# Performance work log

Measured on AMD Instinct MI355X. Metric: run time of the kernel, lower is better.

## Reference

```python
import jax, jax.numpy as jnp
import numpy as np

B, S, D = 4, 2048, 1024
H, HD = 16, 64  # n_heads, head_dim (n_kv_heads == n_heads -> n_rep = 1)
WINDOW = 256
ROPE_THETA = 10000.0


def setup_inputs() -> dict:
    key = jax.random.key(0)
    ks = jax.random.split(key, 5)
    x = jax.random.normal(ks[0], (B, S, D), dtype=jnp.float32)
    scale = 0.02
    wq = jax.random.normal(ks[1], (D, D), dtype=jnp.float32) * scale
    wk = jax.random.normal(ks[2], (D, D), dtype=jnp.float32) * scale
    wv = jax.random.normal(ks[3], (D, D), dtype=jnp.float32) * scale
    wo = jax.random.normal(ks[4], (D, D), dtype=jnp.float32) * scale
    # RoPE frequencies: freqs_cis[t, i] = exp(1j * t / theta^(2i/HD)), i in [0, HD/2)
    inv_freq = 1.0 / (ROPE_THETA ** (jnp.arange(0, HD, 2, dtype=jnp.float32) / HD))
    t = jnp.arange(S, dtype=jnp.float32)
    ang = t[:, None] * inv_freq[None, :]  # [S, HD/2]
    return {"x": x, "freqs_cos": jnp.cos(ang), "freqs_sin": jnp.sin(ang),
            "wq": wq, "wk": wk, "wv": wv, "wo": wo}


def _apply_rope(xq, xk, cos, sin):
    # xq/xk: [B, S, H, HD]; cos/sin: [S, HD/2] broadcast as [1, S, 1, HD/2]
    def rot(v):
        vr = v.reshape(*v.shape[:-1], HD // 2, 2)
        v0, v1 = vr[..., 0], vr[..., 1]
        c = cos[None, :, None, :]
        s = sin[None, :, None, :]
        o0 = v0 * c - v1 * s
        o1 = v0 * s + v1 * c
        return jnp.stack([o0, o1], axis=-1).reshape(v.shape)
    return rot(xq), rot(xk)


def reference(x, freqs_cos, freqs_sin, wq, wk, wv, wo):
    b, s, _ = x.shape
    xq = (x @ wq.T).reshape(b, s, H, HD)
    xk = (x @ wk.T).reshape(b, s, H, HD)
    xv = (x @ wv.T).reshape(b, s, H, HD)
    xq, xk = _apply_rope(xq, xk, freqs_cos, freqs_sin)
    # [B, H, S, S] scores
    scores = jnp.einsum('bqhd,bkhd->bhqk', xq, xk) / jnp.sqrt(jnp.float32(HD))
    pos = jnp.arange(s)
    # masked (disallowed) when j > i (future) or i - j >= window
    bad = (pos[None, :] > pos[:, None]) | (pos[:, None] - pos[None, :] >= WINDOW)
    scores = jnp.where(bad[None, None], -jnp.inf, scores)
    attn = jax.nn.softmax(scores.astype(jnp.float32), axis=-1).astype(xq.dtype)
    out = jnp.einsum('bhqk,bkhd->bqhd', attn, xv).reshape(b, s, H * HD)
    return out @ wo.T
```

## Files before the change

kernel.cpp:

```cpp
#include <hip/hip_runtime.h>
#include <hip/hip_bf16.h>


typedef __bf16 bf16_t;
typedef __attribute__((ext_vector_type(8))) __bf16 bf16x8;
typedef __attribute__((ext_vector_type(4))) __bf16 bf16x4;
typedef __attribute__((ext_vector_type(4))) float f32x4;

#define MFMA16(a, b, c) __builtin_amdgcn_mfma_f32_16x16x32_bf16((a), (b), (c), 0, 0, 0)

__device__ __forceinline__ void async16(const void* g, void* l) {
    __builtin_amdgcn_global_load_lds(
        (const __attribute__((address_space(1))) unsigned int*)g,
        (__attribute__((address_space(3))) unsigned int*)l, 16, 0, 0);
}

#define BAR() do { asm volatile("" ::: "memory"); __builtin_amdgcn_s_barrier(); \
                   asm volatile("" ::: "memory"); } while (0)
#define VMC(N) asm volatile("s_waitcnt vmcnt(" #N ")" ::: "memory")

__global__ __launch_bounds__(256) void cvt_kernel(const float* __restrict__ s,
                                                  bf16_t* __restrict__ d, int n) {
    int i = (blockIdx.x * 256 + threadIdx.x) * 8;
    if (i >= n) return;
    float4 a = *(const float4*)(s + i);
    float4 b = *(const float4*)(s + i + 4);
    bf16x8 o;
    o[0] = (bf16_t)a.x; o[1] = (bf16_t)a.y; o[2] = (bf16_t)a.z; o[3] = (bf16_t)a.w;
    o[4] = (bf16_t)b.x; o[5] = (bf16_t)b.y; o[6] = (bf16_t)b.z; o[7] = (bf16_t)b.w;
    *(bf16x8*)(d + i) = o;
}

template <typename OUT>
__global__ __launch_bounds__(512, 2) void gemm256(const bf16_t* __restrict__ A,
                                                  const bf16_t* __restrict__ Bw,
                                                  OUT* __restrict__ C,
                                                  int M, int N, int K) {
    __shared__ __attribute__((aligned(16))) bf16_t As[49152];
    __shared__ __attribute__((aligned(16))) bf16_t Bs[24576];
    const int tid = threadIdx.x;
    const int l = tid & 63, w = tid >> 6;
    const int lr = l & 15, lg = l >> 4;
    const int wr = w >> 1, wc = w & 1;

    const int nwg = gridDim.x * gridDim.y;
    const int flat = blockIdx.y * gridDim.x + blockIdx.x;
    const int swz = (flat & 7) * (nwg >> 3) + (flat >> 3);
    const int bx = swz % gridDim.x, by = swz / gridDim.x;
    const long m0 = (long)by * 256, n0 = (long)bx * 128;
    const int NT = K >> 6;

    int rS[2], cS[2];
#pragma unroll
    for (int i = 0; i < 2; ++i) {
        const int p  = i * 8192 + w * 1024 + l * 16;
        const int pp = p ^ (((p >> 9) & 1) << 5);
        const int st = pp >> 10;
        rS[i] = (st >> 1) * 16 + ((pp >> 6) & 15);
        cS[i] = (st & 1) * 32 + ((pp >> 4) & 3) * 8;
    }
    const bf16_t* aSrc0 = A  + (m0 + rS[0]) * K + cS[0];
    const bf16_t* aSrc1 = A  + (m0 + rS[1]) * K + cS[1];
    const bf16_t* bSrc0 = Bw + (n0 + rS[0]) * K + cS[0];
    const bf16_t* bSrc1 = Bw + (n0 + rS[1]) * K + cS[1];
    const long hK = 128L * K;

    auto stageA = [&](int b, int h, int t) {
        char* d = (char*)As + b * 32768 + h * 16384 + w * 1024;
        const long o = (long)h * hK + (long)t * 64;
        async16(aSrc0 + o, d);
        async16(aSrc1 + o, d + 8192);
    };
    auto stageB = [&](int b, int t) {
        char* d = (char*)Bs + b * 16384 + w * 1024;
        const long o = (long)t * 64;
        async16(bSrc0 + o, d);
        async16(bSrc1 + o, d + 8192);
    };

    f32x4 acc[4][4] = {};
    bf16x8 af[4][2], blo[2][2], bhi[2][2];
    const int swd = (lr & 8) << 2;

    auto loadA = [&](int b) {
#pragma unroll
        for (int mi = 0; mi < 4; ++mi)
#pragma unroll
            for (int ks = 0; ks < 2; ++ks) {
                const int ra = (wr & 1) * 64 + mi * 16 + lr;
                const int off = ((ra >> 4) * 2 + ks) * 1024 + (ra & 15) * 64 + lg * 16;
                af[mi][ks] = *(const bf16x8*)((const char*)As + b * 32768 +
                                              (wr >> 1) * 16384 + (off ^ swd));
            }
    };
    auto loadB = [&](int b, int nh, bf16x8 (&dst)[2][2]) {
#pragma unroll
        for (int nj = 0; nj < 2; ++nj)
#pragma unroll
            for (int ks = 0; ks < 2; ++ks) {
                const int rb = wc * 64 + (nh * 2 + nj) * 16 + lr;
                const int off = ((rb >> 4) * 2 + ks) * 1024 + (rb & 15) * 64 + lg * 16;
                dst[nj][ks] = *(const bf16x8*)((const char*)Bs + b * 16384 +
                                               (off ^ swd));
            }
    };

#define QMM(NH, BF) do {                                                       \
    __builtin_amdgcn_s_setprio(1);                                             \
    _Pragma("unroll")                                                          \
    for (int mi = 0; mi < 4; ++mi) {                                           \
        acc[mi][(NH)*2]   = MFMA16(af[mi][0], (BF)[0][0], acc[mi][(NH)*2]);    \
        acc[mi][(NH)*2]   = MFMA16(af[mi][1], (BF)[0][1], acc[mi][(NH)*2]);    \
        acc[mi][(NH)*2+1] = MFMA16(af[mi][0], (BF)[1][0], acc[mi][(NH)*2+1]);  \
        acc[mi][(NH)*2+1] = MFMA16(af[mi][1], (BF)[1][1], acc[mi][(NH)*2+1]);  \
    }                                                                          \
    __builtin_amdgcn_s_setprio(0);                                             \
} while (0)

    stageA(0, 0, 0); stageA(0, 1, 0); stageB(0, 0);
    stageA(1, 0, 1); stageA(1, 1, 1); stageB(1, 1);
    VMC(6);
    BAR();

    int bc = 0;
#pragma unroll 1
    for (int t = 0; t < NT - 2; ++t) {
        const int bn = (bc + 2 >= 3) ? bc - 1 : bc + 2;
        loadA(bc); loadB(bc, 0, blo); stageA(bn, 0, t + 2); stageA(bn, 1, t + 2);
        BAR(); QMM(0, blo); BAR();
        loadB(bc, 1, bhi); stageB(bn, t + 2);
        BAR(); QMM(1, bhi);
        if (t < NT - 3) { VMC(6); } else { VMC(0); }
        BAR();
        bc = (bc + 1 >= 3) ? 0 : bc + 1;
    }

    {
        loadA(bc); loadB(bc, 0, blo);
        QMM(0, blo);
        loadB(bc, 1, bhi);
        QMM(1, bhi);
        const int b2 = (bc + 1 >= 3) ? 0 : bc + 1;
        loadA(b2); loadB(b2, 0, blo);
        QMM(0, blo);
        loadB(b2, 1, bhi);
        QMM(1, bhi);
    }
#undef QMM

#pragma unroll
    for (int mi = 0; mi < 4; ++mi)
#pragma unroll
        for (int ni = 0; ni < 4; ++ni)
#pragma unroll
            for (int j = 0; j < 4; ++j) {
                long r = m0 + wr * 64 + mi * 16 + lg * 4 + j;
                long c = n0 + wc * 64 + ni * 16 + lr;
                C[r * (long)N + c] = (OUT)acc[mi][ni][j];
            }
}

__global__ __launch_bounds__(256) void rope_reshape(const bf16_t* __restrict__ Cq,
                                                    const float* __restrict__ fcos,
                                                    const float* __restrict__ fsin,
                                                    bf16_t* __restrict__ Qo,
                                                    bf16_t* __restrict__ Ko,
                                                    bf16_t* __restrict__ VT) {
    __shared__ __attribute__((aligned(16))) bf16_t vt[64][72];
    const int blk = blockIdx.x;
    const int st = blk & 31, bh = blk >> 5;
    const int h = bh & 15, b = bh >> 4;
    const int s0 = st << 6;
    const int tid = threadIdx.x;
    const int i = tid >> 2, dq = (tid & 3) << 4;
    const int s = s0 + i;

    const bf16_t* base = Cq + (long)(b * 2048 + s) * 3072 + h * 64 + dq;
    bf16x8 q0v = *(const bf16x8*)(base);
    bf16x8 q1v = *(const bf16x8*)(base + 8);
    bf16x8 k0v = *(const bf16x8*)(base + 1024);
    bf16x8 k1v = *(const bf16x8*)(base + 1032);
    bf16x8 v0v = *(const bf16x8*)(base + 2048);
    bf16x8 v1v = *(const bf16x8*)(base + 2056);

    float cs[8], sn[8];
    {
        const float* cp = fcos + (long)s * 32 + (dq >> 1);
        const float* sp = fsin + (long)s * 32 + (dq >> 1);
        float4 a = *(const float4*)cp, b2 = *(const float4*)(cp + 4);
        float4 c = *(const float4*)sp, d2 = *(const float4*)(sp + 4);
        cs[0]=a.x; cs[1]=a.y; cs[2]=a.z; cs[3]=a.w; cs[4]=b2.x; cs[5]=b2.y; cs[6]=b2.z; cs[7]=b2.w;
        sn[0]=c.x; sn[1]=c.y; sn[2]=c.z; sn[3]=c.w; sn[4]=d2.x; sn[5]=d2.y; sn[6]=d2.z; sn[7]=d2.w;
    }

    auto rope8 = [&](bf16x8 v, int fo) -> bf16x8 {
        bf16x8 o;
#pragma unroll
        for (int p = 0; p < 4; ++p) {
            float v0 = (float)v[2 * p], v1 = (float)v[2 * p + 1];
            float c = cs[fo + p], s2 = sn[fo + p];
            o[2 * p]     = (bf16_t)(v0 * c - v1 * s2);
            o[2 * p + 1] = (bf16_t)(v0 * s2 + v1 * c);
        }
        return o;
    };

    bf16x8 qo0 = rope8(q0v, 0), qo1 = rope8(q1v, 4);
    bf16x8 ko0 = rope8(k0v, 0), ko1 = rope8(k1v, 4);

    const long qaddr = ((long)bh * 2048 + s) * 64 + dq;
    *(bf16x8*)(Qo + qaddr) = qo0;
    *(bf16x8*)(Qo + qaddr + 8) = qo1;
    *(bf16x8*)(Ko + qaddr) = ko0;
    *(bf16x8*)(Ko + qaddr + 8) = ko1;

    *(bf16x8*)&vt[i][dq] = v0v;
    *(bf16x8*)&vt[i][dq + 8] = v1v;
    __syncthreads();
    const int d = tid >> 2, sb = (tid & 3) << 4;
    bf16x8 o0, o1;
#pragma unroll
    for (int j = 0; j < 8; ++j) {
        const int f = ((j & 3) << 1) | ((j >> 2) & 1);
        o0[j] = vt[sb + f][d];
        o1[j] = vt[sb + 8 + f][d];
    }
    const long va = ((long)bh * 64 + d) * 2048 + s0 + sb;
    *(bf16x8*)(VT + va) = o0;
    *(bf16x8*)(VT + va + 8) = o1;
}

__global__ __launch_bounds__(256, 2) void attn_win4(const bf16_t* __restrict__ Q,
                                                    const bf16_t* __restrict__ Kb,
                                                    const bf16_t* __restrict__ VT,
                                                    bf16_t* __restrict__ Ao) {
    __shared__ __attribute__((aligned(16))) bf16_t kld[5 * 4096];
    __shared__ __attribute__((aligned(16))) bf16_t vld[5 * 4096];
    const int raw = blockIdx.x;
    const int mswz = ((raw & 7) << 8) | (raw >> 3);
    const int qt = mswz & 31, bh = mswz >> 5;
    const int h = bh & 15, b = bh >> 4;
    const int l = threadIdx.x & 63, w = threadIdx.x >> 6;
    const int lr = l & 15, lg = l >> 4;
    const int q0 = qt * 64 + w * 16;
    const int q = q0 + lr;
    const int tb = qt - 4;

    const bf16_t* Qp = Q + (long)bh * 2048 * 64;
    const bf16_t* Kp = Kb + (long)bh * 2048 * 64;
    const bf16_t* Vp = VT + (long)bh * 64 * 2048;

#pragma unroll
    for (int u = 0; u < 5; ++u) {
        const int kt = tb + u;
        const int kt64 = (kt < 0 ? 0 : kt) * 64;
#pragma unroll
        for (int part = 0; part < 2; ++part) {
            const int seg = w * 2 + part;
            const int r = seg * 8 + (l >> 3);
            const int sc = (l & 7) ^ ((r >> 1) & 7);
            async16(Kp + (long)(kt64 + r) * 64 + sc * 8,
                    (char*)kld + u * 8192 + seg * 1024);
            async16(Vp + (long)r * 2048 + kt64 + sc * 8,
                    (char*)vld + u * 8192 + seg * 1024);
        }
    }

    const bf16x8 qb0 = *(const bf16x8*)&Qp[q * 64 + lg * 8];
    const bf16x8 qb1 = *(const bf16x8*)&Qp[q * 64 + 32 + lg * 8];

    __syncthreads();

    float mrun = -1000.f, lsum = 0.f;
    f32x4 o0 = {0.f, 0.f, 0.f, 0.f}, o1 = {0.f, 0.f, 0.f, 0.f};
    f32x4 o2 = {0.f, 0.f, 0.f, 0.f}, o3 = {0.f, 0.f, 0.f, 0.f};
    const int swv = (lr >> 1) & 7;

#define QKF(DST, HH, MM)                                                         \
    f32x4 DST; {                                                                 \
        const int row_ = (HH) * 32 + 2 * lr + (MM);                              \
        const int sw_ = (row_ >> 1) & 7;                                         \
        bf16x8 k0_ = *(const bf16x8*)(kbase + row_ * 128 + ((lg ^ sw_) << 4));   \
        bf16x8 k1_ = *(const bf16x8*)(kbase + row_ * 128 + (((4 + lg) ^ sw_) << 4)); \
        f32x4 s_ = {0.f, 0.f, 0.f, 0.f};                                         \
        s_ = MFMA16(k0_, qb0, s_);                                               \
        s_ = MFMA16(k1_, qb1, s_);                                               \
        const int kb_ = k0s + (HH) * 32 + (MM) + lg * 8;                         \
        DST[0] = ((kb_ >= 0) & ((unsigned)(q - kb_) < 256u))         ? s_[0] * 0.125f : -1e30f; \
        DST[1] = ((kb_ + 2 >= 0) & ((unsigned)(q - kb_ - 2) < 256u)) ? s_[1] * 0.125f : -1e30f; \
        DST[2] = ((kb_ + 4 >= 0) & ((unsigned)(q - kb_ - 4) < 256u)) ? s_[2] * 0.125f : -1e30f; \
        DST[3] = ((kb_ + 6 >= 0) & ((unsigned)(q - kb_ - 6) < 256u)) ? s_[3] * 0.125f : -1e30f; \
    }

#define EXV(S_) {                                                                \
        S_[0] = __expf(S_[0] - mnew); S_[1] = __expf(S_[1] - mnew);              \
        S_[2] = __expf(S_[2] - mnew); S_[3] = __expf(S_[3] - mnew);              \
        rs += (S_[0] + S_[1]) + (S_[2] + S_[3]); }

#define PVF(NT, HH, PB) {                                                        \
        bf16x8 va_ = *(const bf16x8*)(vbase + ((NT) * 16 + lr) * 128 +           \
                                      ((((HH) * 4 + lg) ^ swv) << 4));           \
        o##NT = MFMA16(va_, PB, o##NT); }

#pragma unroll
    for (int u = 0; u < 5; ++u) {
        const char* kbase = (const char*)kld + u * 8192;
        const char* vbase = (const char*)vld + u * 8192;
        const int k0s = (tb + u) * 64;

        QKF(sA, 0, 0) QKF(sB, 0, 1) QKF(sC, 1, 0) QKF(sD, 1, 1)

        float tm = fmaxf(fmaxf(fmaxf(sA[0], sA[1]), fmaxf(sA[2], sA[3])),
                         fmaxf(fmaxf(sB[0], sB[1]), fmaxf(sB[2], sB[3])));
        tm = fmaxf(tm, fmaxf(fmaxf(fmaxf(sC[0], sC[1]), fmaxf(sC[2], sC[3])),
                             fmaxf(fmaxf(sD[0], sD[1]), fmaxf(sD[2], sD[3]))));
        tm = fmaxf(tm, __shfl_xor(tm, 16));
        tm = fmaxf(tm, __shfl_xor(tm, 32));
        const float mnew = fmaxf(mrun, tm);
        const float alpha = __expf(mrun - mnew);
        mrun = mnew;

        float rs = 0.f;
        EXV(sA) EXV(sB) EXV(sC) EXV(sD)
        rs += __shfl_xor(rs, 16);
        rs += __shfl_xor(rs, 32);
        lsum = lsum * alpha + rs;

        o0[0] *= alpha; o0[1] *= alpha; o0[2] *= alpha; o0[3] *= alpha;
        o1[0] *= alpha; o1[1] *= alpha; o1[2] *= alpha; o1[3] *= alpha;
        o2[0] *= alpha; o2[1] *= alpha; o2[2] *= alpha; o2[3] *= alpha;
        o3[0] *= alpha; o3[1] *= alpha; o3[2] *= alpha; o3[3] *= alpha;

        bf16x8 pb0, pb1;
        pb0[0] = (bf16_t)sA[0]; pb0[1] = (bf16_t)sA[1]; pb0[2] = (bf16_t)sA[2]; pb0[3] = (bf16_t)sA[3];
        pb0[4] = (bf16_t)sB[0]; pb0[5] = (bf16_t)sB[1]; pb0[6] = (bf16_t)sB[2]; pb0[7] = (bf16_t)sB[3];
        pb1[0] = (bf16_t)sC[0]; pb1[1] = (bf16_t)sC[1]; pb1[2] = (bf16_t)sC[2]; pb1[3] = (bf16_t)sC[3];
        pb1[4] = (bf16_t)sD[0]; pb1[5] = (bf16_t)sD[1]; pb1[6] = (bf16_t)sD[2]; pb1[7] = (bf16_t)sD[3];

        PVF(0, 0, pb0) PVF(1, 0, pb0) PVF(2, 0, pb0) PVF(3, 0, pb0)
        PVF(0, 1, pb1) PVF(1, 1, pb1) PVF(2, 1, pb1) PVF(3, 1, pb1)
    }
#undef QKF
#undef EXV
#undef PVF

    const float rinv = 1.0f / lsum;
    bf16_t* aor = Ao + ((long)(b * 2048) + q) * 1024 + h * 64;
#define EPI(NT, OA_) {                                                           \
        bf16x4 ov_;                                                             \
        ov_[0] = (bf16_t)(OA_[0] * rinv); ov_[1] = (bf16_t)(OA_[1] * rinv);      \
        ov_[2] = (bf16_t)(OA_[2] * rinv); ov_[3] = (bf16_t)(OA_[3] * rinv);      \
        *(bf16x4*)(aor + (NT) * 16 + lg * 4) = ov_; }
    EPI(0, o0) EPI(1, o1) EPI(2, o2) EPI(3, o3)
#undef EPI
}

extern "C" void kernel_launch(void* const* d_in, const int* in_sizes, int n_in,
                              void* d_out, int out_size, void* d_ws, size_t ws_size,
                              hipStream_t stream) {
    (void)in_sizes; (void)n_in; (void)out_size; (void)ws_size;
    const float* x    = (const float*)d_in[0];
    const float* fcos = (const float*)d_in[1];
    const float* fsin = (const float*)d_in[2];
    const float* wq   = (const float*)d_in[3];
    const float* wk   = (const float*)d_in[4];
    const float* wv   = (const float*)d_in[5];
    const float* wo   = (const float*)d_in[6];
    float* out = (float*)d_out;

    char* ws = (char*)d_ws;
    bf16_t* xbf  = (bf16_t*)(ws);
    bf16_t* wqkv = (bf16_t*)(ws + 16777216);
    bf16_t* wobf = (bf16_t*)(ws + 23068672);
    bf16_t* qkvc = (bf16_t*)(ws + 25165824);
    bf16_t* kbuf = (bf16_t*)(ws + 75497472);
    bf16_t* vtb  = (bf16_t*)(ws + 92274688);
    bf16_t* qbuf = xbf;
    bf16_t* aob  = qkvc;

    cvt_kernel<<<4096, 256, 0, stream>>>(x, xbf, 8388608);
    cvt_kernel<<<512, 256, 0, stream>>>(wq, wqkv, 1048576);
    cvt_kernel<<<512, 256, 0, stream>>>(wk, wqkv + 1048576, 1048576);
    cvt_kernel<<<512, 256, 0, stream>>>(wv, wqkv + 2097152, 1048576);
    cvt_kernel<<<512, 256, 0, stream>>>(wo, wobf, 1048576);

    gemm256<bf16_t><<<dim3(24, 32), 512, 0, stream>>>(xbf, wqkv, qkvc, 8192, 3072, 1024);
    rope_reshape<<<2048, 256, 0, stream>>>(qkvc, fcos, fsin, qbuf, kbuf, vtb);
    attn_win4<<<2048, 256, 0, stream>>>(qbuf, kbuf, vtb, aob);
    gemm256<float><<<dim3(8, 32), 512, 0, stream>>>(aob, wobf, out, 8192, 1024, 1024);
}
```

Measured before the change: 147.1 us.

## Add 256x192-tile QKV GEMM kernel with double-buffered LDS pipeline

Adds a new gemm192 kernel that computes 256x192 output tiles using 8 waves in a 2x4 layout, with double-buffered LDS staging and interleaved async loads. It replaces the 256x128-tile gemm256 for the QKV projection, so the grid drops from 768 to 512 workgroups. The intent is to raise per-workgroup data reuse and shape the wave count to match the 256 CUs with fewer tail waves. The cost is more accumulator registers per thread, since it targets one workgroup per CU with 2 waves per EU, and a more complex hand-scheduled pipeline.

New measurement: 143.0 us. 2.8% less time.

```diff
diff --git a/kernel.cpp b/kernel.cpp
--- a/kernel.cpp
+++ b/kernel.cpp
@@ -29,6 +29,144 @@
     o[0] = (bf16_t)a.x; o[1] = (bf16_t)a.y; o[2] = (bf16_t)a.z; o[3] = (bf16_t)a.w;
     o[4] = (bf16_t)b.x; o[5] = (bf16_t)b.y; o[6] = (bf16_t)b.z; o[7] = (bf16_t)b.w;
     *(bf16x8*)(d + i) = o;
+}
+
+template <typename OUT>
+__global__ __launch_bounds__(512, 1) __attribute__((amdgpu_waves_per_eu(2)))
+void gemm192(const bf16_t* __restrict__ A, const bf16_t* __restrict__ Bw,
+             OUT* __restrict__ C, int M, int N, int K) {
+    __shared__ __attribute__((aligned(16))) bf16_t As[32768];
+    __shared__ __attribute__((aligned(16))) bf16_t Bs[24576];
+    const int tid = threadIdx.x;
+    const int l = tid & 63, w = tid >> 6;
+    const int lr = l & 15, lg = l >> 4;
+    const int wr = w >> 2, wc = w & 3;
+
+    const int nwg = gridDim.x * gridDim.y;
+    const int flat = blockIdx.y * gridDim.x + blockIdx.x;
+    const int swz = (flat & 7) * (nwg >> 3) + (flat >> 3);
+    const int bx = swz % gridDim.x, by = swz / gridDim.x;
+    const long m0 = (long)by * 256, n0 = (long)bx * 192;
+    const int NT = K >> 6;
+    const int NI = NT >> 1;
+
+    const int p  = w * 1024 + l * 16;
+    const int pp = p ^ (((p >> 9) & 1) << 5);
+    const int st = pp >> 10;
+    const int rSt = (st >> 1) * 16 + ((pp >> 6) & 15);
+    const int cSt = (st & 1) * 32 + ((pp >> 4) & 3) * 8;
+    const bf16_t* aS = A  + (m0 + rSt) * K + cSt;
+    const bf16_t* bS = Bw + (n0 + rSt) * K + cSt;
+    const long uK = 64L * K;
+
+    auto stageA = [&](int b, int u, int t) {
+        async16(aS + (long)u * uK + (long)t * 64,
+                (char*)As + b * 32768 + u * 8192 + w * 1024);
+    };
+    auto stageB = [&](int b, int u, int t) {
+        async16(bS + (long)u * uK + (long)t * 64,
+                (char*)Bs + b * 24576 + u * 8192 + w * 1024);
+    };
+
+    f32x4 acc[8][3] = {};
+    bf16x8 afX[4], afY[4], bfX[3], bfY[3];
+    const int swd = (lr & 8) << 2;
+
+    auto loadAF = [&](int b, int mh, int ks, bf16x8 (&dst)[4]) {
+#pragma unroll
+        for (int mi = 0; mi < 4; ++mi) {
+            const int off = (wr * 2 + mh) * 8192 + (mi * 2 + ks) * 1024 +
+                            lr * 64 + lg * 16;
+            dst[mi] = *(const bf16x8*)((const char*)As + b * 32768 + (off ^ swd));
+        }
+    };
+    auto loadBF = [&](int b, int ks, bf16x8 (&dst)[3]) {
+#pragma unroll
+        for (int nj = 0; nj < 3; ++nj) {
+            const int rg = wc * 48 + nj * 16 + lr;
+            const int off = (rg >> 6) * 8192 + (((rg >> 4) & 3) * 2 + ks) * 1024 +
+                            lr * 64 + lg * 16;
+            dst[nj] = *(const bf16x8*)((const char*)Bs + b * 24576 + (off ^ swd));
+        }
+    };
+
+#define QMM(MH, AF, BF) do {                                                   \
+    __builtin_amdgcn_s_setprio(1);                                             \
+    _Pragma("unroll")                                                          \
+    for (int mi = 0; mi < 4; ++mi)                                             \
+        _Pragma("unroll")                                                      \
+        for (int nj = 0; nj < 3; ++nj)                                         \
+            acc[(MH)*4+mi][nj] = MFMA16((AF)[mi], (BF)[nj], acc[(MH)*4+mi][nj]); \
+    __builtin_amdgcn_s_setprio(0);                                             \
+} while (0)
+
+    stageA(0, 0, 0); stageA(0, 1, 0); stageA(0, 2, 0); stageA(0, 3, 0);
+    stageB(0, 0, 0); stageB(0, 1, 0); stageB(0, 2, 0);
+    stageB(1, 0, 1); stageB(1, 1, 1); stageB(1, 2, 1);
+    VMC(3);
+    BAR();
+
+#pragma unroll 1
+    for (int it = 0; it < NI - 1; ++it) {
+        const int T = 2 * it;
+        loadAF(0, 0, 0, afX); loadBF(0, 0, bfX);
+        stageA(1, 0, T + 1); stageA(1, 1, T + 1);
+        BAR(); QMM(0, afX, bfX); BAR();
+        loadAF(0, 1, 0, afY);
+        stageA(1, 2, T + 1); stageA(1, 3, T + 1);
+        BAR(); QMM(1, afY, bfX); BAR();
+        loadAF(0, 0, 1, afX); loadBF(0, 1, bfY);
+        BAR(); QMM(0, afX, bfY); BAR();
+        loadAF(0, 1, 1, afY);
+        stageB(0, 0, T + 2);
+        BAR(); QMM(1, afY, bfY); VMC(1); BAR();
+        loadAF(1, 0, 0, afX); loadBF(1, 0, bfX);
+        stageB(0, 1, T + 2); stageB(0, 2, T + 2);
+        BAR(); QMM(0, afX, bfX); BAR();
+        loadAF(1, 1, 0, afY);
+        stageA(0, 0, T + 2); stageA(0, 1, T + 2);
+        BAR(); QMM(1, afY, bfX); BAR();
+        loadAF(1, 0, 1, afX); loadBF(1, 1, bfY);
+        stageA(0, 2, T + 2); stageA(0, 3, T + 2);
+        BAR(); QMM(0, afX, bfY); BAR();
+        loadAF(1, 1, 1, afY);
+        stageB(1, 0, T + 3); stageB(1, 1, T + 3); stageB(1, 2, T + 3);
+        BAR(); QMM(1, afY, bfY); VMC(3); BAR();
+    }
+
+    {
+        loadAF(0, 0, 0, afX); loadBF(0, 0, bfX);
+        stageA(1, 0, NT - 1); stageA(1, 1, NT - 1);
+        BAR(); QMM(0, afX, bfX); BAR();
+        loadAF(0, 1, 0, afY);
+        stageA(1, 2, NT - 1); stageA(1, 3, NT - 1);
+        BAR(); QMM(1, afY, bfX); BAR();
+        loadAF(0, 0, 1, afX); loadBF(0, 1, bfY);
+        BAR(); QMM(0, afX, bfY); BAR();
+        loadAF(0, 1, 1, afY);
+        BAR(); QMM(1, afY, bfY);
+        VMC(0); BAR();
+        loadAF(1, 0, 0, afX); loadBF(1, 0, bfX);
+        QMM(0, afX, bfX);
+        loadAF(1, 1, 0, afY);
+        QMM(1, afY, bfX);
+        loadAF(1, 0, 1, afX); loadBF(1, 1, bfY);
+        QMM(0, afX, bfY);
+        loadAF(1, 1, 1, afY);
+        QMM(1, afY, bfY);
+    }
+#undef QMM
+
+#pragma unroll
+    for (int ai = 0; ai < 8; ++ai)
+#pragma unroll
+        for (int nj = 0; nj < 3; ++nj)
+#pragma unroll
+            for (int j = 0; j < 4; ++j) {
+                long r = m0 + wr * 128 + ai * 16 + lg * 4 + j;
+                long c = n0 + wc * 48 + nj * 16 + lr;
+                C[r * (long)N + c] = (OUT)acc[ai][nj][j];
+            }
 }
 
 template <typename OUT>
@@ -134,7 +272,6 @@
         BAR();
         bc = (bc + 1 >= 3) ? 0 : bc + 1;
     }
-
     {
         loadA(bc); loadB(bc, 0, blo);
         QMM(0, blo);
@@ -384,7 +521,7 @@
     cvt_kernel<<<512, 256, 0, stream>>>(wv, wqkv + 2097152, 1048576);
     cvt_kernel<<<512, 256, 0, stream>>>(wo, wobf, 1048576);
 
-    gemm256<bf16_t><<<dim3(24, 32), 512, 0, stream>>>(xbf, wqkv, qkvc, 8192, 3072, 1024);
+    gemm192<bf16_t><<<dim3(16, 32), 512, 0, stream>>>(xbf, wqkv, qkvc, 8192, 3072, 1024);
     rope_reshape<<<2048, 256, 0, stream>>>(qkvc, fcos, fsin, qbuf, kbuf, vtb);
     attn_win4<<<2048, 256, 0, stream>>>(qbuf, kbuf, vtb, aob);
     gemm256<float><<<dim3(8, 32), 512, 0, stream>>>(aob, wobf, out, 8192, 1024, 1024);
```
